# Kernel optimization log

Hardware: AMD Instinct MI355X
Metric: run time of the kernel (lower is better)

Reference implementation:

```python
import jax, jax.numpy as jnp
import numpy as np

N_NODES = 50000

def setup_inputs() -> dict:
    key = jax.random.key(0)
    ks = jax.random.split(key, 8)
    input_dim, hidden_dim, output_dim = 128, 256, 64
    x = jax.random.normal(ks[0], (N_NODES, input_dim), dtype=jnp.float32)
    edge_index = jax.random.randint(ks[1], (2, 800000), 0, N_NODES, dtype=jnp.int64)
    s1 = 1.0 / np.sqrt(input_dim)
    s2 = 1.0 / np.sqrt(hidden_dim)
    W1 = jax.random.uniform(ks[2], (input_dim, hidden_dim), jnp.float32, -s1, s1)
    b1 = jax.random.uniform(ks[3], (hidden_dim,), jnp.float32, -s1, s1)
    W2 = jax.random.uniform(ks[4], (hidden_dim, hidden_dim), jnp.float32, -s2, s2)
    b2 = jax.random.uniform(ks[5], (hidden_dim,), jnp.float32, -s2, s2)
    Wc = jax.random.uniform(ks[6], (hidden_dim, output_dim), jnp.float32, -s2, s2)
    bc = jax.random.uniform(ks[7], (output_dim,), jnp.float32, -s2, s2)
    return {"x": x, "edge_index": edge_index, "W1": W1, "b1": b1,
            "W2": W2, "b2": b2, "Wc": Wc, "bc": bc}

def reference(x, edge_index, W1, b1, W2, b2, Wc, bc):
    src, dst = edge_index[0], edge_index[1]
    # GINConv (eps=0): h_i = (1+eps)*x_i + sum_{j->i} x_j
    aggr = jax.ops.segment_sum(x[src], dst, num_segments=N_NODES)  # [N, d_in]
    h = x + aggr
    # 2-layer MLP: Linear -> ReLU -> Linear
    h = jax.nn.relu(h @ W1 + b1) @ W2 + b2  # [N, hidden]
    # classifier on ReLU(conv output)
    return jax.nn.relu(h) @ Wc + bc  # [N, out]
```

## Files before the change

### kernel.cpp

```cpp
#include <hip/hip_runtime.h>
#include <hip/hip_bf16.h>

#define N_NODES 50000
#define M_PAD   50048
#define N_EDGES 800000
#define NBUCK   391
#define NB_EB8  196
#define NB_CAST 3125
#define NB_TR   448
#define EBMAX   4096

typedef __bf16 bf16x8 __attribute__((ext_vector_type(8)));
typedef float  f32x4  __attribute__((ext_vector_type(4)));

__device__ __forceinline__ ushort f2bf(float f) {
    __hip_bfloat16 h = __float2bfloat16(f);
    return __builtin_bit_cast(ushort, h);
}
__device__ __forceinline__ float bf2f(ushort u) {
    return __builtin_bit_cast(float, (unsigned)u << 16);
}

__device__ __forceinline__ void gload16(const ushort* g, ushort* l) {
    __builtin_amdgcn_global_load_lds(
        (const __attribute__((address_space(1))) unsigned*)g,
        (__attribute__((address_space(3))) unsigned*)l, 16, 0, 0);
}

__device__ __forceinline__ void transpose_one(const float* W, ushort* WT,
                                              int K, int N, int t) {
    int k = t / N, n = t % N;
    WT[n * K + k] = f2bf(W[t]);
}

__global__ __launch_bounds__(256) void k_prep(const float* __restrict__ x,
                                              ushort* __restrict__ xb,
                                              const float* __restrict__ W1, ushort* __restrict__ W1T,
                                              const float* __restrict__ W2, ushort* __restrict__ W2T,
                                              const float* __restrict__ Wc, ushort* __restrict__ WcT,
                                              int* __restrict__ bcur) {
    int b = blockIdx.x, t = threadIdx.x;
    if (b < NB_CAST) {
        int i = b * 256 + t;
        const float4* x4 = (const float4*)x;
        float4 a = x4[(size_t)i * 2], bb = x4[(size_t)i * 2 + 1];
        ushort o[8];
        o[0] = f2bf(a.x); o[1] = f2bf(a.y); o[2] = f2bf(a.z); o[3] = f2bf(a.w);
        o[4] = f2bf(bb.x); o[5] = f2bf(bb.y); o[6] = f2bf(bb.z); o[7] = f2bf(bb.w);
        *(uint4*)(xb + (size_t)i * 8) = *(uint4*)o;
    } else if (b < NB_CAST + NB_TR) {
        int tg = (b - NB_CAST) * 256 + t;
        const int S1 = 128 * 256, S2 = 256 * 256, S3 = 256 * 64;
        if (tg < S1) transpose_one(W1, W1T, 128, 256, tg);
        else if (tg < S1 + S2) transpose_one(W2, W2T, 256, 256, tg - S1);
        else if (tg < S1 + S2 + S3) transpose_one(Wc, WcT, 256, 64, tg - S1 - S2);
    } else {
        for (int i = t; i < 400; i += 256) bcur[i] = 0;
    }
}

__global__ __launch_bounds__(512) void k_bscatter(const int* __restrict__ ei,
                                                  int* __restrict__ bcur,
                                                  unsigned* __restrict__ pbuf) {
    __shared__ int lh[NBUCK];
    __shared__ int lbase[NBUCK];
    int t = threadIdx.x;
    for (int i = t; i < NBUCK; i += 512) lh[i] = 0;
    __syncthreads();
    int base = blockIdx.x * 4096 + t;
    int s[8], bk[8], rk[8], lo[8];
#pragma unroll
    for (int k = 0; k < 8; ++k) {
        int e = base + k * 512;
        bool ok = e < N_EDGES;
        int ee = ok ? e : 0;
        s[k] = ei[ee];
        int d = ei[N_EDGES + ee];
        bk[k] = ok ? (d >> 7) : -1;
        lo[k] = d & 127;
    }
#pragma unroll
    for (int k = 0; k < 8; ++k)
        if (bk[k] >= 0) rk[k] = atomicAdd(&lh[bk[k]], 1);
    __syncthreads();
    for (int i = t; i < NBUCK; i += 512) {
        int v = lh[i];
        lbase[i] = v ? atomicAdd(&bcur[i], v) : 0;
    }
    __syncthreads();
#pragma unroll
    for (int k = 0; k < 8; ++k)
        if (bk[k] >= 0) {
            int pos = lbase[bk[k]] + rk[k];
            if (pos < EBMAX)
                pbuf[bk[k] * EBMAX + pos] = (unsigned)s[k] | ((unsigned)lo[k] << 17);
        }
}

__global__ __launch_bounds__(256) void k_bplace(const unsigned* __restrict__ pbuf,
                                                const int* __restrict__ bcur,
                                                int* __restrict__ nodestart,
                                                int* __restrict__ nodecnt,
                                                int* __restrict__ elist) {
    __shared__ int lcnt[128], lexc[128], lcur[128];
    int b = blockIdx.x, t = threadIdx.x;
    int m = bcur[b]; if (m > EBMAX) m = EBMAX;
    const unsigned* pb = pbuf + b * EBMAX;
    if (t < 128) lcnt[t] = 0;
    __syncthreads();
    for (int i = t; i < m; i += 256)
        atomicAdd(&lcnt[pb[i] >> 17], 1);
    __syncthreads();
    if (t < 128) lexc[t] = lcnt[t];
    __syncthreads();
#pragma unroll
    for (int off = 1; off < 128; off <<= 1) {
        int u = (t < 128 && t >= off) ? lexc[t - off] : 0;
        __syncthreads();
        if (t < 128) lexc[t] += u;
        __syncthreads();
    }
    if (t < 128) {
        int e = lexc[t] - lcnt[t];
        int node = (b << 7) + t;
        if (node < N_NODES) {
            nodestart[node] = b * EBMAX + e;
            nodecnt[node] = lcnt[t];
        }
        lcur[t] = e;
    }
    __syncthreads();
    for (int i = t; i < m; i += 256) {
        unsigned pr = pb[i];
        int pos = atomicAdd(&lcur[pr >> 17], 1);
        elist[b * EBMAX + pos] = (int)(pr & 0x1FFFF);
    }
}

__global__ __launch_bounds__(512) void k_fused(const ushort* __restrict__ xb,
                                               const int* __restrict__ nodestart,
                                               const int* __restrict__ nodecnt,
                                               const int* __restrict__ elist,
                                               const ushort* __restrict__ W1T,
                                               const float* __restrict__ b1,
                                               const ushort* __restrict__ W2T,
                                               const float* __restrict__ b2,
                                               const ushort* __restrict__ WcT,
                                               const float* __restrict__ bc,
                                               float* __restrict__ out, int M) {
    __shared__ ushort sA[2][64 * 64];
    __shared__ ushort sB[256 * 64];
    __shared__ ushort ht[64 * 256];

    int m0 = blockIdx.x * 64;
    int tid = threadIdx.x, wv = tid >> 6, lane = tid & 63;
    int lr = lane & 15;
    int kq = (lane >> 4) << 3;
    int l8 = (lane >> 3) & 7, c8 = lane & 7;
    int swz8 = c8 ^ l8;

#pragma unroll
    for (int i = 0; i < 4; ++i) {
        int rg = wv * 32 + i * 8;
        gload16(W1T + (size_t)(rg + l8) * 128 + swz8 * 8, sB + rg * 64);
        gload16(W1T + (size_t)(rg + l8) * 128 + 64 + swz8 * 8, ht + rg * 64);
    }

    {
        int grp = tid >> 4, l16 = tid & 15;
        for (int nd = grp; nd < 64; nd += 32) {
            int node = m0 + nd;
            float a[8];
#pragma unroll
            for (int k = 0; k < 8; ++k) a[k] = 0.0f;
            if (node < N_NODES) {
                uint4 mine = *(const uint4*)(xb + (size_t)node * 128 + l16 * 8);
                const ushort* pm = (const ushort*)&mine;
#pragma unroll
                for (int k = 0; k < 8; ++k) a[k] = bf2f(pm[k]);
                int beg = nodestart[node], cnt = nodecnt[node];
                for (int base = 0; base < cnt; base += 16) {
                    int rem = cnt - base;
                    int idx = (l16 < rem) ? elist[beg + base + l16] : 0;
                    int c = rem < 16 ? rem : 16;
                    int j = 0;
                    for (; j + 8 <= c; j += 8) {
                        uint4 v[8];
#pragma unroll
                        for (int u = 0; u < 8; ++u) {
                            int s = __shfl(idx, j + u, 16);
                            v[u] = *(const uint4*)(xb + (size_t)s * 128 + l16 * 8);
                        }
#pragma unroll
                        for (int u = 0; u < 8; ++u) {
                            const ushort* pv = (const ushort*)&v[u];
#pragma unroll
                            for (int k = 0; k < 8; ++k) a[k] += bf2f(pv[k]);
                        }
                    }
                    for (; j < c; ++j) {
                        int s = __shfl(idx, j, 16);
                        uint4 v = *(const uint4*)(xb + (size_t)s * 128 + l16 * 8);
                        const ushort* pv = (const ushort*)&v;
#pragma unroll
                        for (int k = 0; k < 8; ++k) a[k] += bf2f(pv[k]);
                    }
                }
            }
            ushort o[8];
#pragma unroll
            for (int k = 0; k < 8; ++k) o[k] = f2bf(a[k]);
            int h = l16 >> 3, cch = l16 & 7;
            *(uint4*)(&sA[h][nd * 64 + ((cch ^ (nd & 7)) << 3)]) = *(uint4*)o;
        }
    }
    __syncthreads();

    int wrow0 = (wv >> 2) * 32;
    int wcol0 = (wv & 3) * 64;
    int crow = (lane >> 4) << 2;

    f32x4 acc[2][4];

#pragma unroll
    for (int m = 0; m < 2; ++m)
#pragma unroll
        for (int n = 0; n < 4; ++n) acc[m][n] = 0;

#pragma unroll
    for (int kbh = 0; kbh < 2; ++kbh) {
        const ushort* asrc = sA[kbh];
        const ushort* bsrc = kbh ? ht : sB;
#pragma unroll
        for (int kk = 0; kk < 64; kk += 32) {
            int cb = (kk + kq) * 2;
            bf16x8 af[2], bfr[4];
#pragma unroll
            for (int m = 0; m < 2; ++m) {
                int r = wrow0 + m * 16 + lr;
                af[m] = __builtin_bit_cast(bf16x8,
                    *(const uint4*)((const char*)asrc + r * 128 + (cb ^ ((r & 7) << 4))));
            }
#pragma unroll
            for (int n = 0; n < 4; ++n) {
                int r = wcol0 + n * 16 + lr;
                bfr[n] = __builtin_bit_cast(bf16x8,
                    *(const uint4*)((const char*)bsrc + r * 128 + (cb ^ ((r & 7) << 4))));
            }
#pragma unroll
            for (int m = 0; m < 2; ++m)
#pragma unroll
                for (int n = 0; n < 4; ++n)
                    acc[m][n] = __builtin_amdgcn_mfma_f32_16x16x32_bf16(
                        af[m], bfr[n], acc[m][n], 0, 0, 0);
        }
    }
    __syncthreads();

#pragma unroll
    for (int n = 0; n < 4; ++n) {
        int col = wcol0 + n * 16 + lr;
        float bv = b1[col];
#pragma unroll
        for (int m = 0; m < 2; ++m) {
#pragma unroll
            for (int r = 0; r < 4; ++r) {
                int row = wrow0 + m * 16 + crow + r;
                int sc = ((((col >> 3) ^ (row & 7)) << 3) | (col & 7));
                ht[row * 256 + sc] = f2bf(fmaxf(acc[m][n][r] + bv, 0.0f));
            }
        }
    }
    __syncthreads();

#pragma unroll
    for (int m = 0; m < 2; ++m)
#pragma unroll
        for (int n = 0; n < 4; ++n) acc[m][n] = 0;

    for (int kb = 0; kb < 256; kb += 64) {
#pragma unroll
        for (int i = 0; i < 4; ++i) {
            int rg = wv * 32 + i * 8;
            gload16(W2T + (size_t)(rg + l8) * 256 + kb + swz8 * 8, sB + rg * 64);
        }
        __syncthreads();
#pragma unroll
        for (int kk = 0; kk < 64; kk += 32) {
            int cc = kb + kk + kq;
            int cb = (kk + kq) * 2;
            bf16x8 af[2], bfr[4];
#pragma unroll
            for (int m = 0; m < 2; ++m) {
                int r = wrow0 + m * 16 + lr;
                af[m] = __builtin_bit_cast(bf16x8,
                    *(const uint4*)(ht + r * 256 + ((((cc >> 3) ^ (r & 7)) << 3))));
            }
#pragma unroll
            for (int n = 0; n < 4; ++n) {
                int r = wcol0 + n * 16 + lr;
                bfr[n] = __builtin_bit_cast(bf16x8,
                    *(const uint4*)((const char*)sB + r * 128 + (cb ^ ((r & 7) << 4))));
            }
#pragma unroll
            for (int m = 0; m < 2; ++m)
#pragma unroll
                for (int n = 0; n < 4; ++n)
                    acc[m][n] = __builtin_amdgcn_mfma_f32_16x16x32_bf16(
                        af[m], bfr[n], acc[m][n], 0, 0, 0);
        }
        __syncthreads();
    }
#pragma unroll
    for (int n = 0; n < 4; ++n) {
        int col = wcol0 + n * 16 + lr;
        float bv = b2[col];
#pragma unroll
        for (int m = 0; m < 2; ++m) {
#pragma unroll
            for (int r = 0; r < 4; ++r) {
                int row = wrow0 + m * 16 + crow + r;
                int sc = ((((col >> 3) ^ (row & 7)) << 3) | (col & 7));
                ht[row * 256 + sc] = f2bf(fmaxf(acc[m][n][r] + bv, 0.0f));
            }
        }
    }
#pragma unroll
    for (int i = 0; i < 4; ++i)
        gload16(WcT + (size_t)(wv * 8 + l8) * 256 + i * 64 + swz8 * 8,
                sB + i * 4096 + wv * 8 * 64);
    __syncthreads();

    f32x4 acc3[2];
#pragma unroll
    for (int n = 0; n < 2; ++n) acc3[n] = 0;
    int mrow0 = (wv & 3) * 16;
    int ncol0 = (wv >> 2) * 32;
    int arow3 = mrow0 + lr;
#pragma unroll
    for (int kb4 = 0; kb4 < 4; ++kb4) {
#pragma unroll
        for (int kk = 0; kk < 64; kk += 32) {
            int cc = kb4 * 64 + kk + kq;
            int cb = (kk + kq) * 2;
            bf16x8 a = __builtin_bit_cast(bf16x8,
                *(const uint4*)(ht + arow3 * 256 + ((((cc >> 3) ^ (arow3 & 7)) << 3))));
#pragma unroll
            for (int n = 0; n < 2; ++n) {
                int r = ncol0 + n * 16 + lr;
                bf16x8 b = __builtin_bit_cast(bf16x8,
                    *(const uint4*)((const char*)sB + kb4 * 8192 + r * 128 +
                                    (cb ^ ((r & 7) << 4))));
                acc3[n] = __builtin_amdgcn_mfma_f32_16x16x32_bf16(a, b, acc3[n], 0, 0, 0);
            }
        }
    }
#pragma unroll
    for (int n = 0; n < 2; ++n) {
        int col = ncol0 + n * 16 + lr;
        float bv = bc[col];
#pragma unroll
        for (int r = 0; r < 4; ++r) {
            int grow = m0 + mrow0 + crow + r;
            if (grow < M) out[(size_t)grow * 64 + col] = acc3[n][r] + bv;
        }
    }
}


extern "C" void kernel_launch(void* const* d_in, const int* in_sizes, int n_in,
                              void* d_out, int out_size, void* d_ws, size_t ws_size,
                              hipStream_t stream) {
    const float* x  = (const float*)d_in[0];
    const int*   ei = (const int*)d_in[1];
    const float* W1 = (const float*)d_in[2];
    const float* b1 = (const float*)d_in[3];
    const float* W2 = (const float*)d_in[4];
    const float* b2 = (const float*)d_in[5];
    const float* Wc = (const float*)d_in[6];
    const float* bc = (const float*)d_in[7];
    float* out = (float*)d_out;

    char* p = (char*)d_ws;
    int* bcur        = (int*)p; p += 400 * 4;
    int* nodestart   = (int*)p; p += M_PAD * 4;
    int* nodecnt     = (int*)p; p += M_PAD * 4;
    unsigned* pbuf   = (unsigned*)p; p += (size_t)NBUCK * EBMAX * 4;
    int* elist       = (int*)p; p += (size_t)NBUCK * EBMAX * 4;
    ushort* W1T = (ushort*)p; p += 256 * 128 * 2;
    ushort* W2T = (ushort*)p; p += 256 * 256 * 2;
    ushort* WcT = (ushort*)p; p += 64 * 256 * 2;
    ushort* xb  = (ushort*)p; p += (size_t)N_NODES * 128 * 2;

    k_prep<<<NB_CAST + NB_TR + 1, 256, 0, stream>>>(x, xb, W1, W1T, W2, W2T, Wc, WcT, bcur);
    k_bscatter<<<NB_EB8, 512, 0, stream>>>(ei, bcur, pbuf);
    k_bplace<<<NBUCK, 256, 0, stream>>>(pbuf, bcur, nodestart, nodecnt, elist);
    k_fused<<<M_PAD / 64, 512, 0, stream>>>(xb, nodestart, nodecnt, elist,
                                            W1T, b1, W2T, b2, WcT, bc, out, N_NODES);
}
```

Baseline: 96.27 us.

## Fold edge bucketing into prep kernel with fixed slots; widen fused kernel to 1024 threads

Moves the edge-bucket scatter into the prep kernel. Each scatter block now writes into fixed per-(bucket,block) slots of capacity 32 instead of reserving space with global atomics, which removes one kernel launch and the global atomic counter. The placement kernel reads the per-slot counts and walks the slotted buffer. The fused GNN kernel doubles to 1024 threads per block, so each thread handles one node's aggregation and each wave gets a smaller MMA tile. This trades per-wave work for more parallelism. Slot overflow beyond 32 would drop edges, which is a correctness risk only if the edge distribution is skewed.

```diff
diff --git a/kernel.cpp b/kernel.cpp
--- a/kernel.cpp
+++ b/kernel.cpp
@@ -5,9 +5,10 @@
 #define M_PAD   50048
 #define N_EDGES 800000
 #define NBUCK   391
-#define NB_EB8  196
+#define NB_SC   196
 #define NB_CAST 3125
 #define NB_TR   448
+#define CAP     32
 #define EBMAX   4096
 
 typedef __bf16 bf16x8 __attribute__((ext_vector_type(8)));
@@ -38,7 +39,9 @@
                                               const float* __restrict__ W1, ushort* __restrict__ W1T,
                                               const float* __restrict__ W2, ushort* __restrict__ W2T,
                                               const float* __restrict__ Wc, ushort* __restrict__ WcT,
-                                              int* __restrict__ bcur) {
+                                              const int* __restrict__ ei,
+                                              int* __restrict__ cnt,
+                                              unsigned* __restrict__ pbuf) {
     int b = blockIdx.x, t = threadIdx.x;
     if (b < NB_CAST) {
         int i = b * 256 + t;
@@ -55,61 +58,52 @@
         else if (tg < S1 + S2) transpose_one(W2, W2T, 256, 256, tg - S1);
         else if (tg < S1 + S2 + S3) transpose_one(Wc, WcT, 256, 64, tg - S1 - S2);
     } else {
-        for (int i = t; i < 400; i += 256) bcur[i] = 0;
-    }
-}
-
-__global__ __launch_bounds__(512) void k_bscatter(const int* __restrict__ ei,
-                                                  int* __restrict__ bcur,
-                                                  unsigned* __restrict__ pbuf) {
-    __shared__ int lh[NBUCK];
-    __shared__ int lbase[NBUCK];
-    int t = threadIdx.x;
-    for (int i = t; i < NBUCK; i += 512) lh[i] = 0;
-    __syncthreads();
-    int base = blockIdx.x * 4096 + t;
-    int s[8], bk[8], rk[8], lo[8];
-#pragma unroll
-    for (int k = 0; k < 8; ++k) {
-        int e = base + k * 512;
-        bool ok = e < N_EDGES;
-        int ee = ok ? e : 0;
-        s[k] = ei[ee];
-        int d = ei[N_EDGES + ee];
-        bk[k] = ok ? (d >> 7) : -1;
-        lo[k] = d & 127;
-    }
-#pragma unroll
-    for (int k = 0; k < 8; ++k)
-        if (bk[k] >= 0) rk[k] = atomicAdd(&lh[bk[k]], 1);
-    __syncthreads();
-    for (int i = t; i < NBUCK; i += 512) {
-        int v = lh[i];
-        lbase[i] = v ? atomicAdd(&bcur[i], v) : 0;
-    }
-    __syncthreads();
-#pragma unroll
-    for (int k = 0; k < 8; ++k)
-        if (bk[k] >= 0) {
-            int pos = lbase[bk[k]] + rk[k];
-            if (pos < EBMAX)
-                pbuf[bk[k] * EBMAX + pos] = (unsigned)s[k] | ((unsigned)lo[k] << 17);
-        }
+        __shared__ int lh[NBUCK];
+        int blk = b - NB_CAST - NB_TR;
+        for (int i = t; i < NBUCK; i += 256) lh[i] = 0;
+        __syncthreads();
+        int base = blk * 4096;
+        int s[16], bk[16], rk[16], lo[16];
+#pragma unroll
+        for (int k = 0; k < 16; ++k) {
+            int e = base + k * 256 + t;
+            bool ok = e < N_EDGES;
+            int ee = ok ? e : 0;
+            s[k] = ei[ee];
+            int d = ei[N_EDGES + ee];
+            bk[k] = ok ? (d >> 7) : -1;
+            lo[k] = d & 127;
+        }
+#pragma unroll
+        for (int k = 0; k < 16; ++k)
+            if (bk[k] >= 0) rk[k] = atomicAdd(&lh[bk[k]], 1);
+        __syncthreads();
+        for (int i = t; i < NBUCK; i += 256)
+            cnt[blk * NBUCK + i] = lh[i] < CAP ? lh[i] : CAP;
+#pragma unroll
+        for (int k = 0; k < 16; ++k)
+            if (bk[k] >= 0 && rk[k] < CAP)
+                pbuf[(bk[k] * NB_SC + blk) * CAP + rk[k]] =
+                    (unsigned)s[k] | ((unsigned)lo[k] << 17);
+    }
 }
 
 __global__ __launch_bounds__(256) void k_bplace(const unsigned* __restrict__ pbuf,
-                                                const int* __restrict__ bcur,
+                                                const int* __restrict__ cnt,
                                                 int* __restrict__ nodestart,
                                                 int* __restrict__ nodecnt,
                                                 int* __restrict__ elist) {
     __shared__ int lcnt[128], lexc[128], lcur[128];
+    __shared__ int lcc[NB_SC];
     int b = blockIdx.x, t = threadIdx.x;
-    int m = bcur[b]; if (m > EBMAX) m = EBMAX;
-    const unsigned* pb = pbuf + b * EBMAX;
+    for (int i = t; i < NB_SC; i += 256) lcc[i] = cnt[i * NBUCK + b];
     if (t < 128) lcnt[t] = 0;
     __syncthreads();
-    for (int i = t; i < m; i += 256)
-        atomicAdd(&lcnt[pb[i] >> 17], 1);
+    const unsigned* pb = pbuf + (size_t)b * NB_SC * CAP;
+    for (int i = t; i < NB_SC * CAP; i += 256) {
+        int r = i >> 5, j = i & (CAP - 1);
+        if (j < lcc[r]) atomicAdd(&lcnt[pb[i] >> 17], 1);
+    }
     __syncthreads();
     if (t < 128) lexc[t] = lcnt[t];
     __syncthreads();
@@ -130,24 +124,27 @@
         lcur[t] = e;
     }
     __syncthreads();
-    for (int i = t; i < m; i += 256) {
-        unsigned pr = pb[i];
-        int pos = atomicAdd(&lcur[pr >> 17], 1);
-        elist[b * EBMAX + pos] = (int)(pr & 0x1FFFF);
-    }
-}
-
-__global__ __launch_bounds__(512) void k_fused(const ushort* __restrict__ xb,
-                                               const int* __restrict__ nodestart,
-                                               const int* __restrict__ nodecnt,
-                                               const int* __restrict__ elist,
-                                               const ushort* __restrict__ W1T,
-                                               const float* __restrict__ b1,
-                                               const ushort* __restrict__ W2T,
-                                               const float* __restrict__ b2,
-                                               const ushort* __restrict__ WcT,
-                                               const float* __restrict__ bc,
-                                               float* __restrict__ out, int M) {
+    for (int i = t; i < NB_SC * CAP; i += 256) {
+        int r = i >> 5, j = i & (CAP - 1);
+        if (j < lcc[r]) {
+            unsigned pr = pb[i];
+            int pos = atomicAdd(&lcur[pr >> 17], 1);
+            elist[b * EBMAX + pos] = (int)(pr & 0x1FFFF);
+        }
+    }
+}
+
+__global__ __launch_bounds__(1024, 8) void k_fused(const ushort* __restrict__ xb,
+                                                   const int* __restrict__ nodestart,
+                                                   const int* __restrict__ nodecnt,
+                                                   const int* __restrict__ elist,
+                                                   const ushort* __restrict__ W1T,
+                                                   const float* __restrict__ b1,
+                                                   const ushort* __restrict__ W2T,
+                                                   const float* __restrict__ b2,
+                                                   const ushort* __restrict__ WcT,
+                                                   const float* __restrict__ bc,
+                                                   float* __restrict__ out, int M) {
     __shared__ ushort sA[2][64 * 64];
     __shared__ ushort sB[256 * 64];
     __shared__ ushort ht[64 * 256];
@@ -160,72 +157,70 @@
     int swz8 = c8 ^ l8;
 
 #pragma unroll
-    for (int i = 0; i < 4; ++i) {
-        int rg = wv * 32 + i * 8;
+    for (int i = 0; i < 2; ++i) {
+        int rg = wv * 16 + i * 8;
         gload16(W1T + (size_t)(rg + l8) * 128 + swz8 * 8, sB + rg * 64);
         gload16(W1T + (size_t)(rg + l8) * 128 + 64 + swz8 * 8, ht + rg * 64);
     }
 
     {
-        int grp = tid >> 4, l16 = tid & 15;
-        for (int nd = grp; nd < 64; nd += 32) {
-            int node = m0 + nd;
-            float a[8];
-#pragma unroll
-            for (int k = 0; k < 8; ++k) a[k] = 0.0f;
-            if (node < N_NODES) {
-                uint4 mine = *(const uint4*)(xb + (size_t)node * 128 + l16 * 8);
-                const ushort* pm = (const ushort*)&mine;
-#pragma unroll
-                for (int k = 0; k < 8; ++k) a[k] = bf2f(pm[k]);
-                int beg = nodestart[node], cnt = nodecnt[node];
-                for (int base = 0; base < cnt; base += 16) {
-                    int rem = cnt - base;
-                    int idx = (l16 < rem) ? elist[beg + base + l16] : 0;
-                    int c = rem < 16 ? rem : 16;
-                    int j = 0;
-                    for (; j + 8 <= c; j += 8) {
-                        uint4 v[8];
-#pragma unroll
-                        for (int u = 0; u < 8; ++u) {
-                            int s = __shfl(idx, j + u, 16);
-                            v[u] = *(const uint4*)(xb + (size_t)s * 128 + l16 * 8);
-                        }
-#pragma unroll
-                        for (int u = 0; u < 8; ++u) {
-                            const ushort* pv = (const ushort*)&v[u];
-#pragma unroll
-                            for (int k = 0; k < 8; ++k) a[k] += bf2f(pv[k]);
-                        }
+        int nd = tid >> 4, l16 = tid & 15;
+        int node = m0 + nd;
+        float a[8];
+#pragma unroll
+        for (int k = 0; k < 8; ++k) a[k] = 0.0f;
+        if (node < N_NODES) {
+            uint4 mine = *(const uint4*)(xb + (size_t)node * 128 + l16 * 8);
+            const ushort* pm = (const ushort*)&mine;
+#pragma unroll
+            for (int k = 0; k < 8; ++k) a[k] = bf2f(pm[k]);
+            int beg = nodestart[node], cnt = nodecnt[node];
+            for (int base = 0; base < cnt; base += 16) {
+                int rem = cnt - base;
+                int idx = (l16 < rem) ? elist[beg + base + l16] : 0;
+                int c = rem < 16 ? rem : 16;
+                int j = 0;
+                for (; j + 8 <= c; j += 8) {
+                    uint4 v[8];
+#pragma unroll
+                    for (int u = 0; u < 8; ++u) {
+                        int s = __shfl(idx, j + u, 16);
+                        v[u] = *(const uint4*)(xb + (size_t)s * 128 + l16 * 8);
                     }
-                    for (; j < c; ++j) {
-                        int s = __shfl(idx, j, 16);
-                        uint4 v = *(const uint4*)(xb + (size_t)s * 128 + l16 * 8);
-                        const ushort* pv = (const ushort*)&v;
+#pragma unroll
+                    for (int u = 0; u < 8; ++u) {
+                        const ushort* pv = (const ushort*)&v[u];
 #pragma unroll
                         for (int k = 0; k < 8; ++k) a[k] += bf2f(pv[k]);
                     }
                 }
-            }
-            ushort o[8];
-#pragma unroll
-            for (int k = 0; k < 8; ++k) o[k] = f2bf(a[k]);
-            int h = l16 >> 3, cch = l16 & 7;
-            *(uint4*)(&sA[h][nd * 64 + ((cch ^ (nd & 7)) << 3)]) = *(uint4*)o;
-        }
-    }
-    __syncthreads();
-
-    int wrow0 = (wv >> 2) * 32;
-    int wcol0 = (wv & 3) * 64;
+                for (; j < c; ++j) {
+                    int s = __shfl(idx, j, 16);
+                    uint4 v = *(const uint4*)(xb + (size_t)s * 128 + l16 * 8);
+                    const ushort* pv = (const ushort*)&v;
+#pragma unroll
+                    for (int k = 0; k < 8; ++k) a[k] += bf2f(pv[k]);
+                }
+            }
+        }
+        ushort o[8];
+#pragma unroll
+        for (int k = 0; k < 8; ++k) o[k] = f2bf(a[k]);
+        int h = l16 >> 3, cch = l16 & 7;
+        *(uint4*)(&sA[h][nd * 64 + ((cch ^ (nd & 7)) << 3)]) = *(uint4*)o;
+    }
+    __syncthreads();
+
+    int wrow0 = (wv >> 3) * 32;
+    int wcol0 = (wv & 7) * 32;
     int crow = (lane >> 4) << 2;
 
-    f32x4 acc[2][4];
+    f32x4 acc[2][2];
 
 #pragma unroll
     for (int m = 0; m < 2; ++m)
 #pragma unroll
-        for (int n = 0; n < 4; ++n) acc[m][n] = 0;
+        for (int n = 0; n < 2; ++n) acc[m][n] = 0;
 
 #pragma unroll
     for (int kbh = 0; kbh < 2; ++kbh) {
@@ -234,7 +229,7 @@
 #pragma unroll
         for (int kk = 0; kk < 64; kk += 32) {
             int cb = (kk + kq) * 2;
-            bf16x8 af[2], bfr[4];
+            bf16x8 af[2], bfr[2];
 #pragma unroll
             for (int m = 0; m < 2; ++m) {
                 int r = wrow0 + m * 16 + lr;
@@ -242,7 +237,7 @@
                     *(const uint4*)((const char*)asrc + r * 128 + (cb ^ ((r & 7) << 4))));
             }
 #pragma unroll
-            for (int n = 0; n < 4; ++n) {
+            for (int n = 0; n < 2; ++n) {
                 int r = wcol0 + n * 16 + lr;
                 bfr[n] = __builtin_bit_cast(bf16x8,
                     *(const uint4*)((const char*)bsrc + r * 128 + (cb ^ ((r & 7) << 4))));
@@ -250,7 +245,7 @@
 #pragma unroll
             for (int m = 0; m < 2; ++m)
 #pragma unroll
-                for (int n = 0; n < 4; ++n)
+                for (int n = 0; n < 2; ++n)
                     acc[m][n] = __builtin_amdgcn_mfma_f32_16x16x32_bf16(
                         af[m], bfr[n], acc[m][n], 0, 0, 0);
         }
@@ -258,7 +253,7 @@
     __syncthreads();
 
 #pragma unroll
-    for (int n = 0; n < 4; ++n) {
+    for (int n = 0; n < 2; ++n) {
         int col = wcol0 + n * 16 + lr;
         float bv = b1[col];
 #pragma unroll
@@ -276,12 +271,12 @@
 #pragma unroll
     for (int m = 0; m < 2; ++m)
 #pragma unroll
-        for (int n = 0; n < 4; ++n) acc[m][n] = 0;
+        for (int n = 0; n < 2; ++n) acc[m][n] = 0;
 
     for (int kb = 0; kb < 256; kb += 64) {
 #pragma unroll
-        for (int i = 0; i < 4; ++i) {
-            int rg = wv * 32 + i * 8;
+        for (int i = 0; i < 2; ++i) {
+            int rg = wv * 16 + i * 8;
             gload16(W2T + (size_t)(rg + l8) * 256 + kb + swz8 * 8, sB + rg * 64);
         }
         __syncthreads();
@@ -289,7 +284,7 @@
         for (int kk = 0; kk < 64; kk += 32) {
             int cc = kb + kk + kq;
             int cb = (kk + kq) * 2;
-            bf16x8 af[2], bfr[4];
+            bf16x8 af[2], bfr[2];
 #pragma unroll
             for (int m = 0; m < 2; ++m) {
                 int r = wrow0 + m * 16 + lr;
@@ -297,7 +292,7 @@
                     *(const uint4*)(ht + r * 256 + ((((cc >> 3) ^ (r & 7)) << 3))));
             }
 #pragma unroll
-            for (int n = 0; n < 4; ++n) {
+            for (int n = 0; n < 2; ++n) {
                 int r = wcol0 + n * 16 + lr;
                 bfr[n] = __builtin_bit_cast(bf16x8,
                     *(const uint4*)((const char*)sB + r * 128 + (cb ^ ((r & 7) << 4))));
@@ -305,14 +300,14 @@
 #pragma unroll
             for (int m = 0; m < 2; ++m)
 #pragma unroll
-                for (int n = 0; n < 4; ++n)
+                for (int n = 0; n < 2; ++n)
                     acc[m][n] = __builtin_amdgcn_mfma_f32_16x16x32_bf16(
                         af[m], bfr[n], acc[m][n], 0, 0, 0);
         }
         __syncthreads();
     }
 #pragma unroll
-    for (int n = 0; n < 4; ++n) {
+    for (int n = 0; n < 2; ++n) {
         int col = wcol0 + n * 16 + lr;
         float bv = b2[col];
 #pragma unroll
@@ -325,17 +320,21 @@
             }
         }
     }
-#pragma unroll
-    for (int i = 0; i < 4; ++i)
-        gload16(WcT + (size_t)(wv * 8 + l8) * 256 + i * 64 + swz8 * 8,
-                sB + i * 4096 + wv * 8 * 64);
-    __syncthreads();
-
-    f32x4 acc3[2];
-#pragma unroll
-    for (int n = 0; n < 2; ++n) acc3[n] = 0;
+    {
+        int c = wv >> 2, o = wv & 3;
+#pragma unroll
+        for (int i = 0; i < 2; ++i) {
+            int r0 = (o + i * 4) * 8;
+            gload16(WcT + (size_t)(r0 + l8) * 256 + c * 64 + swz8 * 8,
+                    sB + c * 4096 + r0 * 64);
+        }
+    }
+    __syncthreads();
+
+    f32x4 acc3;
+    acc3 = 0;
     int mrow0 = (wv & 3) * 16;
-    int ncol0 = (wv >> 2) * 32;
+    int ncol0 = (wv >> 2) * 16;
     int arow3 = mrow0 + lr;
 #pragma unroll
     for (int kb4 = 0; kb4 < 4; ++kb4) {
@@ -345,24 +344,20 @@
             int cb = (kk + kq) * 2;
             bf16x8 a = __builtin_bit_cast(bf16x8,
                 *(const uint4*)(ht + arow3 * 256 + ((((cc >> 3) ^ (arow3 & 7)) << 3))));
-#pragma unroll
-            for (int n = 0; n < 2; ++n) {
-                int r = ncol0 + n * 16 + lr;
-                bf16x8 b = __builtin_bit_cast(bf16x8,
-                    *(const uint4*)((const char*)sB + kb4 * 8192 + r * 128 +
-                                    (cb ^ ((r & 7) << 4))));
-                acc3[n] = __builtin_amdgcn_mfma_f32_16x16x32_bf16(a, b, acc3[n], 0, 0, 0);
-            }
-        }
-    }
-#pragma unroll
-    for (int n = 0; n < 2; ++n) {
-        int col = ncol0 + n * 16 + lr;
+            int r = ncol0 + lr;
+            bf16x8 b = __builtin_bit_cast(bf16x8,
+                *(const uint4*)((const char*)sB + kb4 * 8192 + r * 128 +
+                                (cb ^ ((r & 7) << 4))));
+            acc3 = __builtin_amdgcn_mfma_f32_16x16x32_bf16(a, b, acc3, 0, 0, 0);
+        }
+    }
+    {
+        int col = ncol0 + lr;
         float bv = bc[col];
 #pragma unroll
         for (int r = 0; r < 4; ++r) {
             int grow = m0 + mrow0 + crow + r;
-            if (grow < M) out[(size_t)grow * 64 + col] = acc3[n][r] + bv;
+            if (grow < M) out[(size_t)grow * 64 + col] = acc3[r] + bv;
         }
     }
 }
@@ -382,19 +377,19 @@
     float* out = (float*)d_out;
 
     char* p = (char*)d_ws;
-    int* bcur        = (int*)p; p += 400 * 4;
+    int* cnt         = (int*)p; p += NB_SC * NBUCK * 4;
     int* nodestart   = (int*)p; p += M_PAD * 4;
     int* nodecnt     = (int*)p; p += M_PAD * 4;
-    unsigned* pbuf   = (unsigned*)p; p += (size_t)NBUCK * EBMAX * 4;
+    unsigned* pbuf   = (unsigned*)p; p += (size_t)NBUCK * NB_SC * CAP * 4;
     int* elist       = (int*)p; p += (size_t)NBUCK * EBMAX * 4;
     ushort* W1T = (ushort*)p; p += 256 * 128 * 2;
     ushort* W2T = (ushort*)p; p += 256 * 256 * 2;
     ushort* WcT = (ushort*)p; p += 64 * 256 * 2;
     ushort* xb  = (ushort*)p; p += (size_t)N_NODES * 128 * 2;
 
-    k_prep<<<NB_CAST + NB_TR + 1, 256, 0, stream>>>(x, xb, W1, W1T, W2, W2T, Wc, WcT, bcur);
-    k_bscatter<<<NB_EB8, 512, 0, stream>>>(ei, bcur, pbuf);
-    k_bplace<<<NBUCK, 256, 0, stream>>>(pbuf, bcur, nodestart, nodecnt, elist);
-    k_fused<<<M_PAD / 64, 512, 0, stream>>>(xb, nodestart, nodecnt, elist,
-                                            W1T, b1, W2T, b2, WcT, bc, out, N_NODES);
-}
+    k_prep<<<NB_CAST + NB_TR + NB_SC, 256, 0, stream>>>(x, xb, W1, W1T, W2, W2T,
+                                                        Wc, WcT, ei, cnt, pbuf);
+    k_bplace<<<NBUCK, 256, 0, stream>>>(pbuf, cnt, nodestart, nodecnt, elist);
+    k_fused<<<M_PAD / 64, 1024, 0, stream>>>(xb, nodestart, nodecnt, elist,
+                                             W1T, b1, W2T, b2, WcT, bc, out, N_NODES);
+}
```

Result: slower. 108.8 us (+13.0%).

## Fold edge bucketing into prep kernel with per-block segments instead of global atomics

Applied to the files above, without the earlier changes.

Moves the edge bucket-scatter into the prep kernel as extra blocks, which removes one kernel launch. Each scatter block now does a local prefix sum and writes its edges into its own 4096-slot region of the buffer, grouped by bucket, and records per-bucket counts and offsets, so no global atomics are needed. The placement kernel gathers each bucket's pieces from all 196 segments, checking up to 64 slots per segment. This adds more looping and scattered reads in the placement kernel. It also assumes no block puts more than 64 edges into a single bucket; edges beyond that are silently dropped.

```diff
diff --git a/kernel.cpp b/kernel.cpp
--- a/kernel.cpp
+++ b/kernel.cpp
@@ -5,10 +5,11 @@
 #define M_PAD   50048
 #define N_EDGES 800000
 #define NBUCK   391
-#define NB_EB8  196
-#define NB_CAST 3125
-#define NB_TR   448
+#define NB_SC   196
+#define NB_CAST5 1563
+#define NB_TR5  224
 #define EBMAX   4096
+#define MAXSEG  64
 
 typedef __bf16 bf16x8 __attribute__((ext_vector_type(8)));
 typedef float  f32x4  __attribute__((ext_vector_type(4)));
@@ -33,83 +34,97 @@
     WT[n * K + k] = f2bf(W[t]);
 }
 
-__global__ __launch_bounds__(256) void k_prep(const float* __restrict__ x,
+__global__ __launch_bounds__(512) void k_prep(const float* __restrict__ x,
                                               ushort* __restrict__ xb,
                                               const float* __restrict__ W1, ushort* __restrict__ W1T,
                                               const float* __restrict__ W2, ushort* __restrict__ W2T,
                                               const float* __restrict__ Wc, ushort* __restrict__ WcT,
-                                              int* __restrict__ bcur) {
+                                              const int* __restrict__ ei,
+                                              int* __restrict__ cnt,
+                                              int* __restrict__ ofs,
+                                              unsigned* __restrict__ pbuf) {
     int b = blockIdx.x, t = threadIdx.x;
-    if (b < NB_CAST) {
-        int i = b * 256 + t;
-        const float4* x4 = (const float4*)x;
-        float4 a = x4[(size_t)i * 2], bb = x4[(size_t)i * 2 + 1];
-        ushort o[8];
-        o[0] = f2bf(a.x); o[1] = f2bf(a.y); o[2] = f2bf(a.z); o[3] = f2bf(a.w);
-        o[4] = f2bf(bb.x); o[5] = f2bf(bb.y); o[6] = f2bf(bb.z); o[7] = f2bf(bb.w);
-        *(uint4*)(xb + (size_t)i * 8) = *(uint4*)o;
-    } else if (b < NB_CAST + NB_TR) {
-        int tg = (b - NB_CAST) * 256 + t;
+    if (b < NB_CAST5) {
+        int i = b * 512 + t;
+        if (i < N_NODES * 128 / 8) {
+            const float4* x4 = (const float4*)x;
+            float4 a = x4[(size_t)i * 2], bb = x4[(size_t)i * 2 + 1];
+            ushort o[8];
+            o[0] = f2bf(a.x); o[1] = f2bf(a.y); o[2] = f2bf(a.z); o[3] = f2bf(a.w);
+            o[4] = f2bf(bb.x); o[5] = f2bf(bb.y); o[6] = f2bf(bb.z); o[7] = f2bf(bb.w);
+            *(uint4*)(xb + (size_t)i * 8) = *(uint4*)o;
+        }
+    } else if (b < NB_CAST5 + NB_TR5) {
+        int tg = (b - NB_CAST5) * 512 + t;
         const int S1 = 128 * 256, S2 = 256 * 256, S3 = 256 * 64;
         if (tg < S1) transpose_one(W1, W1T, 128, 256, tg);
         else if (tg < S1 + S2) transpose_one(W2, W2T, 256, 256, tg - S1);
         else if (tg < S1 + S2 + S3) transpose_one(Wc, WcT, 256, 64, tg - S1 - S2);
     } else {
-        for (int i = t; i < 400; i += 256) bcur[i] = 0;
-    }
-}
-
-__global__ __launch_bounds__(512) void k_bscatter(const int* __restrict__ ei,
-                                                  int* __restrict__ bcur,
-                                                  unsigned* __restrict__ pbuf) {
-    __shared__ int lh[NBUCK];
-    __shared__ int lbase[NBUCK];
-    int t = threadIdx.x;
-    for (int i = t; i < NBUCK; i += 512) lh[i] = 0;
-    __syncthreads();
-    int base = blockIdx.x * 4096 + t;
-    int s[8], bk[8], rk[8], lo[8];
-#pragma unroll
-    for (int k = 0; k < 8; ++k) {
-        int e = base + k * 512;
-        bool ok = e < N_EDGES;
-        int ee = ok ? e : 0;
-        s[k] = ei[ee];
-        int d = ei[N_EDGES + ee];
-        bk[k] = ok ? (d >> 7) : -1;
-        lo[k] = d & 127;
-    }
-#pragma unroll
-    for (int k = 0; k < 8; ++k)
-        if (bk[k] >= 0) rk[k] = atomicAdd(&lh[bk[k]], 1);
-    __syncthreads();
-    for (int i = t; i < NBUCK; i += 512) {
-        int v = lh[i];
-        lbase[i] = v ? atomicAdd(&bcur[i], v) : 0;
-    }
-    __syncthreads();
-#pragma unroll
-    for (int k = 0; k < 8; ++k)
-        if (bk[k] >= 0) {
-            int pos = lbase[bk[k]] + rk[k];
-            if (pos < EBMAX)
-                pbuf[bk[k] * EBMAX + pos] = (unsigned)s[k] | ((unsigned)lo[k] << 17);
-        }
+        __shared__ int lh[NBUCK];
+        __shared__ int lb[NBUCK];
+        __shared__ int ws[512];
+        int blk = b - NB_CAST5 - NB_TR5;
+        for (int i = t; i < NBUCK; i += 512) lh[i] = 0;
+        __syncthreads();
+        int base = blk * 4096;
+        int s[8], bk[8], rk[8], lo[8];
+#pragma unroll
+        for (int k = 0; k < 8; ++k) {
+            int e = base + k * 512 + t;
+            bool ok = e < N_EDGES;
+            int ee = ok ? e : 0;
+            s[k] = ei[ee];
+            int d = ei[N_EDGES + ee];
+            bk[k] = ok ? (d >> 7) : -1;
+            lo[k] = d & 127;
+        }
+#pragma unroll
+        for (int k = 0; k < 8; ++k)
+            if (bk[k] >= 0) rk[k] = atomicAdd(&lh[bk[k]], 1);
+        __syncthreads();
+        ws[t] = (t < NBUCK) ? lh[t] : 0;
+        __syncthreads();
+#pragma unroll
+        for (int off = 1; off < 512; off <<= 1) {
+            int u = (t >= off) ? ws[t - off] : 0;
+            __syncthreads();
+            ws[t] += u;
+            __syncthreads();
+        }
+        if (t < NBUCK) lb[t] = ws[t] - lh[t];
+        __syncthreads();
+        for (int i = t; i < NBUCK; i += 512) {
+            cnt[blk * NBUCK + i] = lh[i];
+            ofs[blk * NBUCK + i] = lb[i];
+        }
+#pragma unroll
+        for (int k = 0; k < 8; ++k)
+            if (bk[k] >= 0)
+                pbuf[base + lb[bk[k]] + rk[k]] = (unsigned)s[k] | ((unsigned)lo[k] << 17);
+    }
 }
 
 __global__ __launch_bounds__(256) void k_bplace(const unsigned* __restrict__ pbuf,
-                                                const int* __restrict__ bcur,
+                                                const int* __restrict__ cnt,
+                                                const int* __restrict__ ofs,
                                                 int* __restrict__ nodestart,
                                                 int* __restrict__ nodecnt,
                                                 int* __restrict__ elist) {
+    __shared__ int segc[NB_SC], sego[NB_SC];
     __shared__ int lcnt[128], lexc[128], lcur[128];
     int b = blockIdx.x, t = threadIdx.x;
-    int m = bcur[b]; if (m > EBMAX) m = EBMAX;
-    const unsigned* pb = pbuf + b * EBMAX;
+    for (int i = t; i < NB_SC; i += 256) {
+        segc[i] = cnt[i * NBUCK + b];
+        sego[i] = ofs[i * NBUCK + b];
+    }
     if (t < 128) lcnt[t] = 0;
     __syncthreads();
-    for (int i = t; i < m; i += 256)
-        atomicAdd(&lcnt[pb[i] >> 17], 1);
+    for (int i = t; i < NB_SC * MAXSEG; i += 256) {
+        int blk = i >> 6, j = i & (MAXSEG - 1);
+        if (j < segc[blk])
+            atomicAdd(&lcnt[pbuf[blk * 4096 + sego[blk] + j] >> 17], 1);
+    }
     __syncthreads();
     if (t < 128) lexc[t] = lcnt[t];
     __syncthreads();
@@ -130,10 +145,13 @@
         lcur[t] = e;
     }
     __syncthreads();
-    for (int i = t; i < m; i += 256) {
-        unsigned pr = pb[i];
-        int pos = atomicAdd(&lcur[pr >> 17], 1);
-        elist[b * EBMAX + pos] = (int)(pr & 0x1FFFF);
+    for (int i = t; i < NB_SC * MAXSEG; i += 256) {
+        int blk = i >> 6, j = i & (MAXSEG - 1);
+        if (j < segc[blk]) {
+            unsigned pr = pbuf[blk * 4096 + sego[blk] + j];
+            int pos = atomicAdd(&lcur[pr >> 17], 1);
+            elist[b * EBMAX + pos] = (int)(pr & 0x1FFFF);
+        }
     }
 }
 
@@ -382,19 +400,20 @@
     float* out = (float*)d_out;
 
     char* p = (char*)d_ws;
-    int* bcur        = (int*)p; p += 400 * 4;
+    int* cnt         = (int*)p; p += NB_SC * NBUCK * 4;
+    int* ofs         = (int*)p; p += NB_SC * NBUCK * 4;
     int* nodestart   = (int*)p; p += M_PAD * 4;
     int* nodecnt     = (int*)p; p += M_PAD * 4;
-    unsigned* pbuf   = (unsigned*)p; p += (size_t)NBUCK * EBMAX * 4;
+    unsigned* pbuf   = (unsigned*)p; p += (size_t)NB_SC * 4096 * 4;
     int* elist       = (int*)p; p += (size_t)NBUCK * EBMAX * 4;
     ushort* W1T = (ushort*)p; p += 256 * 128 * 2;
     ushort* W2T = (ushort*)p; p += 256 * 256 * 2;
     ushort* WcT = (ushort*)p; p += 64 * 256 * 2;
     ushort* xb  = (ushort*)p; p += (size_t)N_NODES * 128 * 2;
 
-    k_prep<<<NB_CAST + NB_TR + 1, 256, 0, stream>>>(x, xb, W1, W1T, W2, W2T, Wc, WcT, bcur);
-    k_bscatter<<<NB_EB8, 512, 0, stream>>>(ei, bcur, pbuf);
-    k_bplace<<<NBUCK, 256, 0, stream>>>(pbuf, bcur, nodestart, nodecnt, elist);
+    k_prep<<<NB_CAST5 + NB_TR5 + NB_SC, 512, 0, stream>>>(x, xb, W1, W1T, W2, W2T,
+                                                          Wc, WcT, ei, cnt, ofs, pbuf);
+    k_bplace<<<NBUCK, 256, 0, stream>>>(pbuf, cnt, ofs, nodestart, nodecnt, elist);
     k_fused<<<M_PAD / 64, 512, 0, stream>>>(xb, nodestart, nodecnt, elist,
                                             W1T, b1, W2T, b2, WcT, bc, out, N_NODES);
 }
```

Result: slower. 118.3 us (+22.8%).

## Halve fused kernel row tile to 32 nodes to raise occupancy

Applied to the files above, without the earlier changes.

Shrinks the fused gather+MLP kernel tile from 64 to 32 nodes per block, halving shared memory (sA, sB, ht) and accumulator registers, and sets launch bounds to allow more resident blocks. Weight tiles are now staged in 128-column halves, adding extra loads and barriers per layer. The aim is more concurrent blocks to hide the irregular gather latency, at the cost of weights being re-read by twice as many blocks and smaller MFMA reuse per wave.

```diff
diff --git a/kernel.cpp b/kernel.cpp
--- a/kernel.cpp
+++ b/kernel.cpp
@@ -137,22 +137,22 @@
     }
 }
 
-__global__ __launch_bounds__(512) void k_fused(const ushort* __restrict__ xb,
-                                               const int* __restrict__ nodestart,
-                                               const int* __restrict__ nodecnt,
-                                               const int* __restrict__ elist,
-                                               const ushort* __restrict__ W1T,
-                                               const float* __restrict__ b1,
-                                               const ushort* __restrict__ W2T,
-                                               const float* __restrict__ b2,
-                                               const ushort* __restrict__ WcT,
-                                               const float* __restrict__ bc,
-                                               float* __restrict__ out, int M) {
-    __shared__ ushort sA[2][64 * 64];
-    __shared__ ushort sB[256 * 64];
-    __shared__ ushort ht[64 * 256];
-
-    int m0 = blockIdx.x * 64;
+__global__ __launch_bounds__(512, 8) void k_fused(const ushort* __restrict__ xb,
+                                                  const int* __restrict__ nodestart,
+                                                  const int* __restrict__ nodecnt,
+                                                  const int* __restrict__ elist,
+                                                  const ushort* __restrict__ W1T,
+                                                  const float* __restrict__ b1,
+                                                  const ushort* __restrict__ W2T,
+                                                  const float* __restrict__ b2,
+                                                  const ushort* __restrict__ WcT,
+                                                  const float* __restrict__ bc,
+                                                  float* __restrict__ out, int M) {
+    __shared__ ushort sA[2][32 * 64];
+    __shared__ ushort sB[128 * 64];
+    __shared__ ushort ht[32 * 256];
+
+    int m0 = blockIdx.x * 32;
     int tid = threadIdx.x, wv = tid >> 6, lane = tid & 63;
     int lr = lane & 15;
     int kq = (lane >> 4) << 3;
@@ -160,209 +160,217 @@
     int swz8 = c8 ^ l8;
 
 #pragma unroll
-    for (int i = 0; i < 4; ++i) {
-        int rg = wv * 32 + i * 8;
+    for (int i = 0; i < 2; ++i) {
+        int rg = wv * 16 + i * 8;
         gload16(W1T + (size_t)(rg + l8) * 128 + swz8 * 8, sB + rg * 64);
-        gload16(W1T + (size_t)(rg + l8) * 128 + 64 + swz8 * 8, ht + rg * 64);
+        gload16(W1T + (size_t)(128 + rg + l8) * 128 + swz8 * 8, ht + rg * 64);
     }
 
     {
-        int grp = tid >> 4, l16 = tid & 15;
-        for (int nd = grp; nd < 64; nd += 32) {
-            int node = m0 + nd;
-            float a[8];
-#pragma unroll
-            for (int k = 0; k < 8; ++k) a[k] = 0.0f;
-            if (node < N_NODES) {
-                uint4 mine = *(const uint4*)(xb + (size_t)node * 128 + l16 * 8);
-                const ushort* pm = (const ushort*)&mine;
-#pragma unroll
-                for (int k = 0; k < 8; ++k) a[k] = bf2f(pm[k]);
-                int beg = nodestart[node], cnt = nodecnt[node];
-                for (int base = 0; base < cnt; base += 16) {
-                    int rem = cnt - base;
-                    int idx = (l16 < rem) ? elist[beg + base + l16] : 0;
-                    int c = rem < 16 ? rem : 16;
-                    int j = 0;
-                    for (; j + 8 <= c; j += 8) {
-                        uint4 v[8];
-#pragma unroll
-                        for (int u = 0; u < 8; ++u) {
-                            int s = __shfl(idx, j + u, 16);
-                            v[u] = *(const uint4*)(xb + (size_t)s * 128 + l16 * 8);
-                        }
-#pragma unroll
-                        for (int u = 0; u < 8; ++u) {
-                            const ushort* pv = (const ushort*)&v[u];
-#pragma unroll
-                            for (int k = 0; k < 8; ++k) a[k] += bf2f(pv[k]);
-                        }
+        int nd = tid >> 4, l16 = tid & 15;
+        int node = m0 + nd;
+        float a[8];
+#pragma unroll
+        for (int k = 0; k < 8; ++k) a[k] = 0.0f;
+        if (node < N_NODES) {
+            uint4 mine = *(const uint4*)(xb + (size_t)node * 128 + l16 * 8);
+            const ushort* pm = (const ushort*)&mine;
+#pragma unroll
+            for (int k = 0; k < 8; ++k) a[k] = bf2f(pm[k]);
+            int beg = nodestart[node], cnt = nodecnt[node];
+            for (int base = 0; base < cnt; base += 16) {
+                int rem = cnt - base;
+                int idx = (l16 < rem) ? elist[beg + base + l16] : 0;
+                int c = rem < 16 ? rem : 16;
+                int j = 0;
+                for (; j + 8 <= c; j += 8) {
+                    uint4 v[8];
+#pragma unroll
+                    for (int u = 0; u < 8; ++u) {
+                        int s = __shfl(idx, j + u, 16);
+                        v[u] = *(const uint4*)(xb + (size_t)s * 128 + l16 * 8);
                     }
-                    for (; j < c; ++j) {
-                        int s = __shfl(idx, j, 16);
-                        uint4 v = *(const uint4*)(xb + (size_t)s * 128 + l16 * 8);
-                        const ushort* pv = (const ushort*)&v;
+#pragma unroll
+                    for (int u = 0; u < 8; ++u) {
+                        const ushort* pv = (const ushort*)&v[u];
 #pragma unroll
                         for (int k = 0; k < 8; ++k) a[k] += bf2f(pv[k]);
                     }
                 }
-            }
-            ushort o[8];
-#pragma unroll
-            for (int k = 0; k < 8; ++k) o[k] = f2bf(a[k]);
-            int h = l16 >> 3, cch = l16 & 7;
-            *(uint4*)(&sA[h][nd * 64 + ((cch ^ (nd & 7)) << 3)]) = *(uint4*)o;
-        }
-    }
-    __syncthreads();
-
-    int wrow0 = (wv >> 2) * 32;
-    int wcol0 = (wv & 3) * 64;
+                for (; j < c; ++j) {
+                    int s = __shfl(idx, j, 16);
+                    uint4 v = *(const uint4*)(xb + (size_t)s * 128 + l16 * 8);
+                    const ushort* pv = (const ushort*)&v;
+#pragma unroll
+                    for (int k = 0; k < 8; ++k) a[k] += bf2f(pv[k]);
+                }
+            }
+        }
+        ushort o[8];
+#pragma unroll
+        for (int k = 0; k < 8; ++k) o[k] = f2bf(a[k]);
+        int h = l16 >> 3, cch = l16 & 7;
+        *(uint4*)(&sA[h][nd * 64 + ((cch ^ (nd & 7)) << 3)]) = *(uint4*)o;
+    }
+    __syncthreads();
+
+    int wrow0 = (wv >> 2) * 16;
+    int wcol0 = (wv & 3) * 32;
     int crow = (lane >> 4) << 2;
 
-    f32x4 acc[2][4];
-
-#pragma unroll
-    for (int m = 0; m < 2; ++m)
-#pragma unroll
-        for (int n = 0; n < 4; ++n) acc[m][n] = 0;
-
-#pragma unroll
-    for (int kbh = 0; kbh < 2; ++kbh) {
-        const ushort* asrc = sA[kbh];
-        const ushort* bsrc = kbh ? ht : sB;
+    f32x4 acc[2][2];
+#pragma unroll
+    for (int h = 0; h < 2; ++h)
+#pragma unroll
+        for (int n = 0; n < 2; ++n) acc[h][n] = 0;
+
+#pragma unroll
+    for (int r01 = 0; r01 < 2; ++r01) {
+        const ushort* bsrc = r01 ? ht : sB;
 #pragma unroll
         for (int kk = 0; kk < 64; kk += 32) {
             int cb = (kk + kq) * 2;
-            bf16x8 af[2], bfr[4];
-#pragma unroll
-            for (int m = 0; m < 2; ++m) {
-                int r = wrow0 + m * 16 + lr;
-                af[m] = __builtin_bit_cast(bf16x8,
-                    *(const uint4*)((const char*)asrc + r * 128 + (cb ^ ((r & 7) << 4))));
-            }
-#pragma unroll
-            for (int n = 0; n < 4; ++n) {
+            int ra = wrow0 + lr;
+            bf16x8 af = __builtin_bit_cast(bf16x8,
+                *(const uint4*)((const char*)sA[0] + ra * 128 + (cb ^ ((ra & 7) << 4))));
+#pragma unroll
+            for (int n = 0; n < 2; ++n) {
                 int r = wcol0 + n * 16 + lr;
-                bfr[n] = __builtin_bit_cast(bf16x8,
+                bf16x8 bf = __builtin_bit_cast(bf16x8,
                     *(const uint4*)((const char*)bsrc + r * 128 + (cb ^ ((r & 7) << 4))));
-            }
-#pragma unroll
-            for (int m = 0; m < 2; ++m)
-#pragma unroll
-                for (int n = 0; n < 4; ++n)
-                    acc[m][n] = __builtin_amdgcn_mfma_f32_16x16x32_bf16(
-                        af[m], bfr[n], acc[m][n], 0, 0, 0);
-        }
-    }
-    __syncthreads();
-
-#pragma unroll
-    for (int n = 0; n < 4; ++n) {
-        int col = wcol0 + n * 16 + lr;
-        float bv = b1[col];
-#pragma unroll
-        for (int m = 0; m < 2; ++m) {
+                acc[r01][n] = __builtin_amdgcn_mfma_f32_16x16x32_bf16(af, bf, acc[r01][n], 0, 0, 0);
+            }
+        }
+    }
+#pragma unroll
+    for (int nh = 0; nh < 2; ++nh) {
+        __syncthreads();
+#pragma unroll
+        for (int i = 0; i < 2; ++i) {
+            int rg = wv * 16 + i * 8;
+            gload16(W1T + (size_t)(nh * 128 + rg + l8) * 128 + 64 + swz8 * 8, sB + rg * 64);
+        }
+        __syncthreads();
+#pragma unroll
+        for (int kk = 0; kk < 64; kk += 32) {
+            int cb = (kk + kq) * 2;
+            int ra = wrow0 + lr;
+            bf16x8 af = __builtin_bit_cast(bf16x8,
+                *(const uint4*)((const char*)sA[1] + ra * 128 + (cb ^ ((ra & 7) << 4))));
+#pragma unroll
+            for (int n = 0; n < 2; ++n) {
+                int r = wcol0 + n * 16 + lr;
+                bf16x8 bf = __builtin_bit_cast(bf16x8,
+                    *(const uint4*)((const char*)sB + r * 128 + (cb ^ ((r & 7) << 4))));
+                acc[nh][n] = __builtin_amdgcn_mfma_f32_16x16x32_bf16(af, bf, acc[nh][n], 0, 0, 0);
+            }
+        }
+    }
+    __syncthreads();
+
+#pragma unroll
+    for (int nh = 0; nh < 2; ++nh) {
+#pragma unroll
+        for (int n = 0; n < 2; ++n) {
+            int col = nh * 128 + wcol0 + n * 16 + lr;
+            float bv = b1[col];
 #pragma unroll
             for (int r = 0; r < 4; ++r) {
-                int row = wrow0 + m * 16 + crow + r;
+                int row = wrow0 + crow + r;
                 int sc = ((((col >> 3) ^ (row & 7)) << 3) | (col & 7));
-                ht[row * 256 + sc] = f2bf(fmaxf(acc[m][n][r] + bv, 0.0f));
-            }
-        }
-    }
-    __syncthreads();
-
-#pragma unroll
-    for (int m = 0; m < 2; ++m)
-#pragma unroll
-        for (int n = 0; n < 4; ++n) acc[m][n] = 0;
+                ht[row * 256 + sc] = f2bf(fmaxf(acc[nh][n][r] + bv, 0.0f));
+            }
+        }
+    }
+    __syncthreads();
+
+#pragma unroll
+    for (int h = 0; h < 2; ++h)
+#pragma unroll
+        for (int n = 0; n < 2; ++n) acc[h][n] = 0;
 
     for (int kb = 0; kb < 256; kb += 64) {
 #pragma unroll
-        for (int i = 0; i < 4; ++i) {
-            int rg = wv * 32 + i * 8;
-            gload16(W2T + (size_t)(rg + l8) * 256 + kb + swz8 * 8, sB + rg * 64);
-        }
-        __syncthreads();
-#pragma unroll
-        for (int kk = 0; kk < 64; kk += 32) {
-            int cc = kb + kk + kq;
-            int cb = (kk + kq) * 2;
-            bf16x8 af[2], bfr[4];
-#pragma unroll
-            for (int m = 0; m < 2; ++m) {
-                int r = wrow0 + m * 16 + lr;
-                af[m] = __builtin_bit_cast(bf16x8,
-                    *(const uint4*)(ht + r * 256 + ((((cc >> 3) ^ (r & 7)) << 3))));
-            }
-#pragma unroll
-            for (int n = 0; n < 4; ++n) {
-                int r = wcol0 + n * 16 + lr;
-                bfr[n] = __builtin_bit_cast(bf16x8,
-                    *(const uint4*)((const char*)sB + r * 128 + (cb ^ ((r & 7) << 4))));
-            }
-#pragma unroll
-            for (int m = 0; m < 2; ++m)
-#pragma unroll
-                for (int n = 0; n < 4; ++n)
-                    acc[m][n] = __builtin_amdgcn_mfma_f32_16x16x32_bf16(
-                        af[m], bfr[n], acc[m][n], 0, 0, 0);
-        }
-        __syncthreads();
-    }
-#pragma unroll
-    for (int n = 0; n < 4; ++n) {
-        int col = wcol0 + n * 16 + lr;
-        float bv = b2[col];
-#pragma unroll
-        for (int m = 0; m < 2; ++m) {
+        for (int nh = 0; nh < 2; ++nh) {
+#pragma unroll
+            for (int i = 0; i < 2; ++i) {
+                int rg = wv * 16 + i * 8;
+                gload16(W2T + (size_t)(nh * 128 + rg + l8) * 256 + kb + swz8 * 8, sB + rg * 64);
+            }
+            __syncthreads();
+#pragma unroll
+            for (int kk = 0; kk < 64; kk += 32) {
+                int cc = kb + kk + kq;
+                int cb = (kk + kq) * 2;
+                int ra = wrow0 + lr;
+                bf16x8 af = __builtin_bit_cast(bf16x8,
+                    *(const uint4*)(ht + ra * 256 + ((((cc >> 3) ^ (ra & 7)) << 3))));
+#pragma unroll
+                for (int n = 0; n < 2; ++n) {
+                    int r = wcol0 + n * 16 + lr;
+                    bf16x8 bf = __builtin_bit_cast(bf16x8,
+                        *(const uint4*)((const char*)sB + r * 128 + (cb ^ ((r & 7) << 4))));
+                    acc[nh][n] = __builtin_amdgcn_mfma_f32_16x16x32_bf16(af, bf, acc[nh][n], 0, 0, 0);
+                }
+            }
+            __syncthreads();
+        }
+    }
+
+#pragma unroll
+    for (int nh = 0; nh < 2; ++nh) {
+#pragma unroll
+        for (int n = 0; n < 2; ++n) {
+            int col = nh * 128 + wcol0 + n * 16 + lr;
+            float bv = b2[col];
 #pragma unroll
             for (int r = 0; r < 4; ++r) {
-                int row = wrow0 + m * 16 + crow + r;
+                int row = wrow0 + crow + r;
                 int sc = ((((col >> 3) ^ (row & 7)) << 3) | (col & 7));
-                ht[row * 256 + sc] = f2bf(fmaxf(acc[m][n][r] + bv, 0.0f));
-            }
-        }
-    }
-#pragma unroll
-    for (int i = 0; i < 4; ++i)
-        gload16(WcT + (size_t)(wv * 8 + l8) * 256 + i * 64 + swz8 * 8,
-                sB + i * 4096 + wv * 8 * 64);
-    __syncthreads();
-
-    f32x4 acc3[2];
-#pragma unroll
-    for (int n = 0; n < 2; ++n) acc3[n] = 0;
-    int mrow0 = (wv & 3) * 16;
-    int ncol0 = (wv >> 2) * 32;
-    int arow3 = mrow0 + lr;
-#pragma unroll
-    for (int kb4 = 0; kb4 < 4; ++kb4) {
-#pragma unroll
-        for (int kk = 0; kk < 64; kk += 32) {
-            int cc = kb4 * 64 + kk + kq;
-            int cb = (kk + kq) * 2;
-            bf16x8 a = __builtin_bit_cast(bf16x8,
-                *(const uint4*)(ht + arow3 * 256 + ((((cc >> 3) ^ (arow3 & 7)) << 3))));
-#pragma unroll
-            for (int n = 0; n < 2; ++n) {
-                int r = ncol0 + n * 16 + lr;
+                ht[row * 256 + sc] = f2bf(fmaxf(acc[nh][n][r] + bv, 0.0f));
+            }
+        }
+    }
+
+    f32x4 acc3;
+    acc3 = 0;
+    int mrow0 = (wv & 1) * 16;
+    int ncol0 = (wv >> 1) * 16;
+#pragma unroll
+    for (int kh = 0; kh < 2; ++kh) {
+        __syncthreads();
+        {
+            int rg = wv * 8;
+#pragma unroll
+            for (int c = 0; c < 2; ++c)
+                gload16(WcT + (size_t)(rg + l8) * 256 + kh * 128 + c * 64 + swz8 * 8,
+                        sB + c * 4096 + rg * 64);
+        }
+        __syncthreads();
+#pragma unroll
+        for (int lc = 0; lc < 2; ++lc) {
+#pragma unroll
+            for (int kk = 0; kk < 64; kk += 32) {
+                int cc = (kh * 2 + lc) * 64 + kk + kq;
+                int cb = (kk + kq) * 2;
+                int ra = mrow0 + lr;
+                bf16x8 a = __builtin_bit_cast(bf16x8,
+                    *(const uint4*)(ht + ra * 256 + ((((cc >> 3) ^ (ra & 7)) << 3))));
+                int r = ncol0 + lr;
                 bf16x8 b = __builtin_bit_cast(bf16x8,
-                    *(const uint4*)((const char*)sB + kb4 * 8192 + r * 128 +
+                    *(const uint4*)((const char*)sB + lc * 8192 + r * 128 +
                                     (cb ^ ((r & 7) << 4))));
-                acc3[n] = __builtin_amdgcn_mfma_f32_16x16x32_bf16(a, b, acc3[n], 0, 0, 0);
-            }
-        }
-    }
-#pragma unroll
-    for (int n = 0; n < 2; ++n) {
-        int col = ncol0 + n * 16 + lr;
+                acc3 = __builtin_amdgcn_mfma_f32_16x16x32_bf16(a, b, acc3, 0, 0, 0);
+            }
+        }
+    }
+    {
+        int col = ncol0 + lr;
         float bv = bc[col];
 #pragma unroll
         for (int r = 0; r < 4; ++r) {
             int grow = m0 + mrow0 + crow + r;
-            if (grow < M) out[(size_t)grow * 64 + col] = acc3[n][r] + bv;
+            if (grow < M) out[(size_t)grow * 64 + col] = acc3[r] + bv;
         }
     }
 }
@@ -395,6 +403,6 @@
     k_prep<<<NB_CAST + NB_TR + 1, 256, 0, stream>>>(x, xb, W1, W1T, W2, W2T, Wc, WcT, bcur);
     k_bscatter<<<NB_EB8, 512, 0, stream>>>(ei, bcur, pbuf);
     k_bplace<<<NBUCK, 256, 0, stream>>>(pbuf, bcur, nodestart, nodecnt, elist);
-    k_fused<<<M_PAD / 64, 512, 0, stream>>>(xb, nodestart, nodecnt, elist,
+    k_fused<<<M_PAD / 32, 512, 0, stream>>>(xb, nodestart, nodecnt, elist,
                                             W1T, b1, W2T, b2, WcT, bc, out, N_NODES);
 }
```

After: 100.6 us. 4.5% more time.
